# Performance work log

Measured on AMD Instinct MI355X. Metric: run time of the kernel, lower is better.

Reference implementation:

```python
import jax, jax.numpy as jnp
import numpy as np

B, CQ, CM, K, O = 8, 128, 128, 128, 128
LQ, LK = 2048, 2048


def setup_inputs() -> dict:
    key = jax.random.key(0)
    ks = jax.random.split(key, 8)
    s = 0.05
    return {
        "x1": jax.random.normal(ks[0], (B, CQ, LQ), dtype=jnp.float32),
        "x2": jax.random.normal(ks[1], (B, CM, LK), dtype=jnp.float32),
        "Wq": jax.random.normal(ks[2], (K, CQ), dtype=jnp.float32) * s,
        "bq": jax.random.normal(ks[3], (K,), dtype=jnp.float32) * s,
        "Wk": jax.random.normal(ks[4], (K, CM), dtype=jnp.float32) * s,
        "bk": jax.random.normal(ks[5], (K,), dtype=jnp.float32) * s,
        "Wv": jax.random.normal(ks[6], (O, CM), dtype=jnp.float32) * s,
        "bv": jax.random.normal(ks[7], (O,), dtype=jnp.float32) * s,
    }


def reference(x1, x2, Wq, bq, Wk, bk, Wv, bv):
    # Conv1d with kernel_size=1 == per-position linear over channels
    q = jnp.einsum("bcq,kc->bkq", x1, Wq) + bq[None, :, None]  # (B,K,Lq)
    k = jnp.einsum("bcm,kc->bkm", x2, Wk) + bk[None, :, None]  # (B,K,Lk)
    v = jnp.einsum("bcm,oc->bom", x2, Wv) + bv[None, :, None]  # (B,O,Lk)
    # u[b,m,q] = sum_k q[b,k,q]*k[b,k,m] / sqrt(K)   -> (B,Lk,Lq)
    scale = 1.0 / np.sqrt(q.shape[1]).astype(np.float32)
    u = jnp.einsum("bkq,bkm->bmq", q, k) * scale
    w = jax.nn.softmax(u, axis=1)  # softmax over Lk (torch dim=1)
    # out[b,o,q] = sum_m w[b,m,q]*v[b,o,m]   -> (B,O,Lq)
    out = jnp.einsum("bmq,bom->boq", w, v)
    return (out, w)
```

## Files before the change

kernel.cpp:

```cpp
#include <hip/hip_runtime.h>
#include <cstddef>

#define B_ 8
#define C_ 128
#define K_ 128
#define L_ 2048

static constexpr float SCALE = 0.08838834764831843f;

typedef unsigned short u16;
typedef __attribute__((ext_vector_type(8))) short bf16x8;
typedef __attribute__((ext_vector_type(4))) unsigned short u16x4;
typedef __attribute__((ext_vector_type(4))) unsigned int u32x4;
typedef __attribute__((ext_vector_type(4))) float f32x4;
typedef __attribute__((ext_vector_type(16))) float f32x16;

__device__ __forceinline__ u16 f2bf(float x) {
    unsigned u = __builtin_bit_cast(unsigned, x);
    u += 0x7FFFu + ((u >> 16) & 1u);
    return (u16)(u >> 16);
}

__device__ __forceinline__ unsigned cvtpk(float lo, float hi) {
    unsigned r;
    asm("v_cvt_pk_bf16_f32 %0, %1, %2" : "=v"(r) : "v"(lo), "v"(hi));
    return r;
}
__device__ __forceinline__ void plswap(unsigned& a, unsigned& b) {
    asm volatile("v_permlane32_swap_b32 %0, %1" : "+v"(a), "+v"(b));
}

#define MFMA32 __builtin_amdgcn_mfma_f32_32x32x16_bf16


__global__ __launch_bounds__(256) void xpose_kernel(
    const float* __restrict__ x1, const float* __restrict__ x2,
    u16* __restrict__ xT1, u16* __restrict__ xT2)
{
    const int src = blockIdx.z;
    const int b   = blockIdx.y;
    const int l   = blockIdx.x * 128 + (threadIdx.x & 127);
    const int half = threadIdx.x >> 7;
    const float* X = src ? x2 : x1;
    u16* dst       = src ? xT2 : xT1;
    const float* xb = X + ((size_t)b * C_ + half * 64) * L_ + l;
    u16* db = dst + ((size_t)b * L_ + l) * C_ + half * 64;
    for (int c0 = 0; c0 < 64; c0 += 8) {
        bf16x8 pk;
        #pragma unroll
        for (int j = 0; j < 8; ++j)
            pk[j] = (short)f2bf(xb[(size_t)(c0 + j) * L_]);
        *(bf16x8*)(db + c0) = pk;
    }
}

__global__ __launch_bounds__(256) void proj_kernel(
    const u16* __restrict__ xT1, const u16* __restrict__ xT2,
    const float* __restrict__ Wq, const float* __restrict__ bq,
    const float* __restrict__ Wk, const float* __restrict__ bk,
    const float* __restrict__ Wv, const float* __restrict__ bv,
    u16* __restrict__ qF, u16* __restrict__ kF, u16* __restrict__ vF)
{
    const int l0 = blockIdx.x * 64;
    const int p  = blockIdx.y % 3;
    const int b  = blockIdx.y / 3;
    const float* W    = (p == 0) ? Wq : (p == 1) ? Wk : Wv;
    const float* bias = (p == 0) ? bq : (p == 1) ? bk : bv;
    const u16* xT     = (p == 0) ? xT1 : xT2;

    __shared__ u16 Wls[128 * 136];
    const int tid = threadIdx.x;
    for (int i = tid; i < 4096; i += 256) {
        float4 v = ((const float4*)W)[i];
        int e = i << 2; int row = e >> 7; int colc = e & 127;
        u16x4 pk = { f2bf(v.x), f2bf(v.y), f2bf(v.z), f2bf(v.w) };
        *(u16x4*)&Wls[row * 136 + colc] = pk;
    }
    __syncthreads();

    const int w = tid >> 6, l = tid & 63;
    const int lr = l & 15, lg = l >> 4;
    const int lrow = l0 + w * 16 + lr;

    bf16x8 xfr[4];
    const u16* xb = xT + ((size_t)b * L_ + lrow) * C_;
    #pragma unroll
    for (int s = 0; s < 4; ++s)
        xfr[s] = *(const bf16x8*)(xb + s * 32 + lg * 8);

    const int hl2 = lg >> 1, j0 = (lg & 1) * 4;

    for (int kt = 0; kt < 8; ++kt) {
        bf16x8 wfr[4];
        #pragma unroll
        for (int s = 0; s < 4; ++s)
            wfr[s] = *(const bf16x8*)&Wls[(kt * 16 + lr) * 136 + s * 32 + lg * 8];
        f32x4 acc = {0.f, 0.f, 0.f, 0.f};
        if (p < 2) {
            #pragma unroll
            for (int s = 0; s < 4; ++s)
                acc = __builtin_amdgcn_mfma_f32_16x16x32_bf16(wfr[s], xfr[s], acc, 0, 0, 0);
            u16x4 pk;
            #pragma unroll
            for (int r = 0; r < 4; ++r)
                pk[r] = f2bf(acc[r] + bias[kt * 16 + lg * 4 + r]);
            const int qt = lrow >> 5, qloc = lrow & 31;
            u16* dstp = ((p == 0) ? qF : kF)
                + (((size_t)b * 64 + qt) * 8 + kt) * 512 + hl2 * 256 + qloc * 8 + j0;
            *(u16x4*)dstp = pk;
        } else {
            #pragma unroll
            for (int s = 0; s < 4; ++s)
                acc = __builtin_amdgcn_mfma_f32_16x16x32_bf16(xfr[s], wfr[s], acc, 0, 0, 0);
            const int o = kt * 16 + lr;
            const float bo = bias[o];
            u16x4 pk;
            #pragma unroll
            for (int r = 0; r < 4; ++r)
                pk[r] = f2bf(acc[r] + bo);
            const int mt  = (l0 >> 5) + ((w * 16 + lg * 4) >> 5);
            const int t   = w & 1;
            const int ob  = kt >> 1;
            const int oloc = (kt & 1) * 16 + lr;
            u16* dstp = vF + ((size_t)b * 64 + mt) * 4096
                + ob * 1024 + t * 512 + hl2 * 256 + oloc * 8 + j0;
            *(u16x4*)dstp = pk;
        }
    }
}

__global__ __launch_bounds__(512, 2) void fused_attn_kernel(
    const u16* __restrict__ qF, const u16* __restrict__ kF,
    const u16* __restrict__ vF, float* __restrict__ out,
    float* __restrict__ wout)
{
    __shared__ float red[4 * 128 * 32];
    __shared__ float cred[8 * 32];

    const int bid = blockIdx.x;
    const int b   = bid & 7;
    const int qt  = bid >> 3;
    const int q0  = qt * 32;
    const int tid = threadIdx.x;
    const int w   = tid >> 6;
    const int l   = tid & 63;
    const int col = l & 31;
    const int hl  = l >> 5;

    bf16x8 qf[8];
    {
        const u16* qp = qF + (((size_t)b * 64 + qt) * 8) * 512 + l * 8;
        #pragma unroll
        for (int ks = 0; ks < 8; ++ks)
            qf[ks] = *(const bf16x8*)(qp + ks * 512);
    }

    const u16* kbase = kF + (((size_t)b * 64 + w * 8) * 8) * 512 + l * 8;
    const u16* vbase = vF + ((size_t)b * 64 + w * 8) * 4096 + l * 8;

    u32x4 ePA[8], ePB[8];
    float csum = 0.f;

    bf16x8 kA[8], kB[8];
    auto LK = [&](bf16x8 (&d)[8], int it) {
        const u16* ka = kbase + (size_t)it * 4096;
        #pragma unroll
        for (int j = 0; j < 8; ++j)
            d[j] = *(const bf16x8*)(ka + j * 512);
    };

    LK(kA, 0);
    #pragma unroll
    for (int it = 0; it < 8; ++it) {
        bf16x8* kf = (it & 1) ? kB : kA;
        bf16x8 (&kn)[8] = (it & 1) ? kA : kB;
        f32x16 sa = {}, sb = {};
        sa = MFMA32(kf[0], qf[0], sa, 0, 0, 0); sb = MFMA32(kf[4], qf[4], sb, 0, 0, 0);
        sa = MFMA32(kf[1], qf[1], sa, 0, 0, 0); sb = MFMA32(kf[5], qf[5], sb, 0, 0, 0);
        sa = MFMA32(kf[2], qf[2], sa, 0, 0, 0); sb = MFMA32(kf[6], qf[6], sb, 0, 0, 0);
        sa = MFMA32(kf[3], qf[3], sa, 0, 0, 0); sb = MFMA32(kf[7], qf[7], sb, 0, 0, 0);
        if (it < 7) LK(kn, it + 1);

        float e[16];
        #pragma unroll
        for (int r = 0; r < 16; ++r)
            e[r] = __expf((sa[r] + sb[r]) * SCALE);
        float c0 = (e[0] + e[1]) + (e[2] + e[3]);
        float c1 = (e[4] + e[5]) + (e[6] + e[7]);
        float c2 = (e[8] + e[9]) + (e[10] + e[11]);
        float c3 = (e[12] + e[13]) + (e[14] + e[15]);
        csum += (c0 + c1) + (c2 + c3);

        unsigned R0 = cvtpk(e[0], e[1]),   R1 = cvtpk(e[2], e[3]);
        unsigned R2 = cvtpk(e[4], e[5]),   R3 = cvtpk(e[6], e[7]);
        unsigned R4 = cvtpk(e[8], e[9]),   R5 = cvtpk(e[10], e[11]);
        unsigned R6 = cvtpk(e[12], e[13]), R7 = cvtpk(e[14], e[15]);
        plswap(R0, R2); plswap(R1, R3); plswap(R4, R6); plswap(R5, R7);
        ePA[it] = u32x4{ R0, R1, R2, R3 };
        ePB[it] = u32x4{ R4, R5, R6, R7 };
    }

    csum += __shfl_xor(csum, 32);
    if (hl == 0) cred[w * 32 + col] = csum;
    __syncthreads();
    const float rs = 1.0f / (((cred[col]       + cred[32 + col])
                            + (cred[64 + col]  + cred[96 + col]))
                           + ((cred[128 + col] + cred[160 + col])
                            + (cred[192 + col] + cred[224 + col])));

    f32x16 pv0 = {}, pv1 = {}, pv2 = {}, pv3 = {};

    bf16x8 vA[8], vB[8];
    auto LV = [&](bf16x8 (&d)[8], int it) {
        const u16* va = vbase + (size_t)it * 4096;
        #pragma unroll
        for (int j = 0; j < 8; ++j)
            d[j] = *(const bf16x8*)(va + j * 512);
    };

    LV(vA, 0);
    #pragma unroll
    for (int it = 0; it < 8; ++it) {
        bf16x8* vf = (it & 1) ? vB : vA;
        bf16x8 (&vn)[8] = (it & 1) ? vA : vB;
        if (it < 7) LV(vn, it + 1);

        bf16x8 B0 = __builtin_bit_cast(bf16x8, ePA[it]);
        bf16x8 B1 = __builtin_bit_cast(bf16x8, ePB[it]);

        pv0 = MFMA32(vf[0], B0, pv0, 0, 0, 0); pv1 = MFMA32(vf[2], B0, pv1, 0, 0, 0);
        pv2 = MFMA32(vf[4], B0, pv2, 0, 0, 0); pv3 = MFMA32(vf[6], B0, pv3, 0, 0, 0);
        pv0 = MFMA32(vf[1], B1, pv0, 0, 0, 0); pv1 = MFMA32(vf[3], B1, pv1, 0, 0, 0);
        pv2 = MFMA32(vf[5], B1, pv2, 0, 0, 0); pv3 = MFMA32(vf[7], B1, pv3, 0, 0, 0);

        float* wp = wout + ((size_t)b * L_ + w * 256 + it * 32 + hl * 8) * L_ + q0 + col;
        #pragma unroll
        for (int d = 0; d < 4; ++d) {
            const unsigned da = ePA[it][d], db = ePB[it][d];
            wp[(size_t)(2 * d) * L_]
                = __builtin_bit_cast(float, da << 16) * rs;
            wp[(size_t)(2 * d + 1) * L_]
                = __builtin_bit_cast(float, da & 0xFFFF0000u) * rs;
            wp[(size_t)(16 + 2 * d) * L_]
                = __builtin_bit_cast(float, db << 16) * rs;
            wp[(size_t)(16 + 2 * d + 1) * L_]
                = __builtin_bit_cast(float, db & 0xFFFF0000u) * rs;
        }
    }

    if (w >= 4) {
        float* rp = red + (size_t)(w - 4) * 128 * 32 + col;
        #pragma unroll
        for (int g = 0; g < 4; ++g)
            #pragma unroll
            for (int rr = 0; rr < 4; ++rr) {
                const int ol = rr + 8 * g + 4 * hl;
                rp[(ol)      * 32] = pv0[4 * g + rr];
                rp[(ol + 32) * 32] = pv1[4 * g + rr];
                rp[(ol + 64) * 32] = pv2[4 * g + rr];
                rp[(ol + 96) * 32] = pv3[4 * g + rr];
            }
    }
    __syncthreads();
    if (w < 4) {
        float* rp = red + (size_t)w * 128 * 32 + col;
        #pragma unroll
        for (int g = 0; g < 4; ++g)
            #pragma unroll
            for (int rr = 0; rr < 4; ++rr) {
                const int ol = rr + 8 * g + 4 * hl;
                rp[(ol)      * 32] += pv0[4 * g + rr];
                rp[(ol + 32) * 32] += pv1[4 * g + rr];
                rp[(ol + 64) * 32] += pv2[4 * g + rr];
                rp[(ol + 96) * 32] += pv3[4 * g + rr];
            }
    }
    __syncthreads();

    {
        const int qq = tid & 31;
        const int og = tid >> 5;
        float* ob = out + ((size_t)b * K_) * L_ + q0 + qq;
        #pragma unroll
        for (int i = 0; i < 8; ++i) {
            const int o = og + 16 * i;
            const float v = red[(0 * 128 + o) * 32 + qq] + red[(1 * 128 + o) * 32 + qq]
                          + red[(2 * 128 + o) * 32 + qq] + red[(3 * 128 + o) * 32 + qq];
            ob[(size_t)o * L_] = v * rs;
        }
    }
}

extern "C" void kernel_launch(void* const* d_in, const int* in_sizes, int n_in,
                              void* d_out, int out_size, void* d_ws, size_t ws_size,
                              hipStream_t stream) {
    (void)in_sizes; (void)n_in; (void)out_size; (void)ws_size;
    const float* x1 = (const float*)d_in[0];
    const float* x2 = (const float*)d_in[1];
    const float* Wq = (const float*)d_in[2];
    const float* bq = (const float*)d_in[3];
    const float* Wk = (const float*)d_in[4];
    const float* bk = (const float*)d_in[5];
    const float* Wv = (const float*)d_in[6];
    const float* bv = (const float*)d_in[7];

    float* out  = (float*)d_out;
    float* wout = out + (size_t)B_ * K_ * L_;

    const size_t NPROJ = (size_t)B_ * L_ * K_;
    u16* qF  = (u16*)d_ws;
    u16* kF  = qF  + NPROJ;
    u16* vF  = kF  + NPROJ;
    u16* xT1 = vF  + NPROJ;
    u16* xT2 = xT1 + NPROJ;

    xpose_kernel<<<dim3(L_ / 128, B_, 2), 256, 0, stream>>>(x1, x2, xT1, xT2);

    proj_kernel<<<dim3(L_ / 64, B_ * 3), 256, 0, stream>>>(
        xT1, xT2, Wq, bq, Wk, bk, Wv, bv, qF, kF, vF);

    fused_attn_kernel<<<dim3(512), 512, 0, stream>>>(qF, kF, vF, out, wout);
}
```

Before: 65.57 us.

## Fuse input transpose into projection kernel and use nontemporal output stores

Removes the separate transpose kernel: the projection kernel now reads fp32 x directly, converts to bf16 and transposes through shared memory before the MFMA loop. This drops a kernel launch and the bf16 workspace round trip. The cost is that x2 is now read twice (once for K, once for V), and the shared-memory writes of single u16 values at stride 136 may cause bank conflicts. Separately, the large softmax-weight and output writes switch to nontemporal stores to reduce cache pollution.

Result: slower. 68.83 us (+5.0%).

```diff
diff --git a/kernel.cpp b/kernel.cpp
--- a/kernel.cpp
+++ b/kernel.cpp
@@ -33,29 +33,8 @@
 #define MFMA32 __builtin_amdgcn_mfma_f32_32x32x16_bf16
 
 
-__global__ __launch_bounds__(256) void xpose_kernel(
+__global__ __launch_bounds__(256) void proj_kernel(
     const float* __restrict__ x1, const float* __restrict__ x2,
-    u16* __restrict__ xT1, u16* __restrict__ xT2)
-{
-    const int src = blockIdx.z;
-    const int b   = blockIdx.y;
-    const int l   = blockIdx.x * 128 + (threadIdx.x & 127);
-    const int half = threadIdx.x >> 7;
-    const float* X = src ? x2 : x1;
-    u16* dst       = src ? xT2 : xT1;
-    const float* xb = X + ((size_t)b * C_ + half * 64) * L_ + l;
-    u16* db = dst + ((size_t)b * L_ + l) * C_ + half * 64;
-    for (int c0 = 0; c0 < 64; c0 += 8) {
-        bf16x8 pk;
-        #pragma unroll
-        for (int j = 0; j < 8; ++j)
-            pk[j] = (short)f2bf(xb[(size_t)(c0 + j) * L_]);
-        *(bf16x8*)(db + c0) = pk;
-    }
-}
-
-__global__ __launch_bounds__(256) void proj_kernel(
-    const u16* __restrict__ xT1, const u16* __restrict__ xT2,
     const float* __restrict__ Wq, const float* __restrict__ bq,
     const float* __restrict__ Wk, const float* __restrict__ bk,
     const float* __restrict__ Wv, const float* __restrict__ bv,
@@ -66,27 +45,40 @@
     const int b  = blockIdx.y / 3;
     const float* W    = (p == 0) ? Wq : (p == 1) ? Wk : Wv;
     const float* bias = (p == 0) ? bq : (p == 1) ? bk : bv;
-    const u16* xT     = (p == 0) ? xT1 : xT2;
+    const float* X    = (p == 0) ? x1 : x2;
 
     __shared__ u16 Wls[128 * 136];
+    __shared__ u16 xls[64 * 136];
     const int tid = threadIdx.x;
+
     for (int i = tid; i < 4096; i += 256) {
         float4 v = ((const float4*)W)[i];
         int e = i << 2; int row = e >> 7; int colc = e & 127;
         u16x4 pk = { f2bf(v.x), f2bf(v.y), f2bf(v.z), f2bf(v.w) };
         *(u16x4*)&Wls[row * 136 + colc] = pk;
     }
+
+    {
+        const int lane = tid & 63;
+        const int crow = tid >> 6;
+        const float* xp = X + ((size_t)b * C_ + crow) * L_ + l0 + lane;
+        #pragma unroll 4
+        for (int c0 = crow; c0 < 128; c0 += 4) {
+            xls[lane * 136 + c0] = f2bf(*xp);
+            xp += 4 * (size_t)L_;
+        }
+    }
     __syncthreads();
 
     const int w = tid >> 6, l = tid & 63;
     const int lr = l & 15, lg = l >> 4;
     const int lrow = l0 + w * 16 + lr;
+    const int lloc = w * 16 + lr;
 
     bf16x8 xfr[4];
-    const u16* xb = xT + ((size_t)b * L_ + lrow) * C_;
     #pragma unroll
     for (int s = 0; s < 4; ++s)
-        xfr[s] = *(const bf16x8*)(xb + s * 32 + lg * 8);
+        xfr[s] = *(const bf16x8*)&xls[lloc * 136 + s * 32 + lg * 8];
 
     const int hl2 = lg >> 1, j0 = (lg & 1) * 4;
 
@@ -237,14 +229,18 @@
         #pragma unroll
         for (int d = 0; d < 4; ++d) {
             const unsigned da = ePA[it][d], db = ePB[it][d];
-            wp[(size_t)(2 * d) * L_]
-                = __builtin_bit_cast(float, da << 16) * rs;
-            wp[(size_t)(2 * d + 1) * L_]
-                = __builtin_bit_cast(float, da & 0xFFFF0000u) * rs;
-            wp[(size_t)(16 + 2 * d) * L_]
-                = __builtin_bit_cast(float, db << 16) * rs;
-            wp[(size_t)(16 + 2 * d + 1) * L_]
-                = __builtin_bit_cast(float, db & 0xFFFF0000u) * rs;
+            __builtin_nontemporal_store(
+                __builtin_bit_cast(float, da << 16) * rs,
+                &wp[(size_t)(2 * d) * L_]);
+            __builtin_nontemporal_store(
+                __builtin_bit_cast(float, da & 0xFFFF0000u) * rs,
+                &wp[(size_t)(2 * d + 1) * L_]);
+            __builtin_nontemporal_store(
+                __builtin_bit_cast(float, db << 16) * rs,
+                &wp[(size_t)(16 + 2 * d) * L_]);
+            __builtin_nontemporal_store(
+                __builtin_bit_cast(float, db & 0xFFFF0000u) * rs,
+                &wp[(size_t)(16 + 2 * d + 1) * L_]);
         }
     }
 
@@ -286,7 +282,7 @@
             const int o = og + 16 * i;
             const float v = red[(0 * 128 + o) * 32 + qq] + red[(1 * 128 + o) * 32 + qq]
                           + red[(2 * 128 + o) * 32 + qq] + red[(3 * 128 + o) * 32 + qq];
-            ob[(size_t)o * L_] = v * rs;
+            __builtin_nontemporal_store(v * rs, &ob[(size_t)o * L_]);
         }
     }
 }
@@ -311,13 +307,9 @@
     u16* qF  = (u16*)d_ws;
     u16* kF  = qF  + NPROJ;
     u16* vF  = kF  + NPROJ;
-    u16* xT1 = vF  + NPROJ;
-    u16* xT2 = xT1 + NPROJ;
-
-    xpose_kernel<<<dim3(L_ / 128, B_, 2), 256, 0, stream>>>(x1, x2, xT1, xT2);
 
     proj_kernel<<<dim3(L_ / 64, B_ * 3), 256, 0, stream>>>(
-        xT1, xT2, Wq, bq, Wk, bk, Wv, bv, qF, kF, vF);
+        x1, x2, Wq, bq, Wk, bk, Wv, bv, qF, kF, vF);
 
     fused_attn_kernel<<<dim3(512), 512, 0, stream>>>(qF, kF, vF, out, wout);
 }
```
